# Kernel tuning notes

Hardware: AMD Instinct MI355X
Metric: run time of the kernel (lower is better)

The kernel has to match this reference:

```python
import jax, jax.numpy as jnp
import numpy as np

D_MODEL = 2048
N_HEAD = 16
HEAD_DIM = D_MODEL // N_HEAD


def setup_inputs() -> dict:
    key = jax.random.key(0)
    k1, k2, k3 = jax.random.split(key, 3)
    B, T = 4, 1024
    x = jax.random.normal(k1, (B, T, D_MODEL), dtype=jnp.float32)
    # Linear(d_model, 3*d_model, bias=False): stored as [in, out] for x @ W
    w_qkv = jax.random.normal(k2, (D_MODEL, 3 * D_MODEL), dtype=jnp.float32) * (1.0 / np.sqrt(D_MODEL))
    w_proj = jax.random.normal(k3, (D_MODEL, D_MODEL), dtype=jnp.float32) * (1.0 / np.sqrt(D_MODEL))
    return {"x": x, "w_qkv": w_qkv, "w_proj": w_proj}


def reference(x, w_qkv, w_proj):
    B, T, C = x.shape
    H, Dh = N_HEAD, HEAD_DIM
    qkv = x @ w_qkv                              # [B, T, 3C]
    q, k, v = jnp.split(qkv, 3, axis=-1)
    # [B, T, C] -> [B, H, T, Dh]
    q = q.reshape(B, T, H, Dh).transpose(0, 2, 1, 3)
    k = k.reshape(B, T, H, Dh).transpose(0, 2, 1, 3)
    v = v.reshape(B, T, H, Dh).transpose(0, 2, 1, 3)
    scale = 1.0 / np.sqrt(Dh).astype(np.float32)
    scores = jnp.einsum('bhqd,bhkd->bhqk', q, k) * scale   # [B, H, T, T]
    causal = jnp.tril(jnp.ones((T, T), dtype=bool))
    scores = jnp.where(causal, scores, jnp.finfo(scores.dtype).min)
    attn = jax.nn.softmax(scores, axis=-1)
    y = jnp.einsum('bhqk,bhkd->bhqd', attn, v)             # [B, H, T, Dh]
    y = y.transpose(0, 2, 1, 3).reshape(B, T, C)
    return y @ w_proj
```

## Files before the change

kernel.cpp:

```cpp
#include <hip/hip_runtime.h>
#include <cstdint>
#include <cstddef>


typedef __attribute__((ext_vector_type(8))) __bf16 bf16x8;
typedef __attribute__((ext_vector_type(4))) float f32x4;
typedef unsigned short u16;

#define NEG_BIG (-1.0e30f)

__device__ __forceinline__ u16 f2bf(float f) {
    union { float f; uint32_t u; } v; v.f = f;
    uint32_t r = v.u + 0x7FFFu + ((v.u >> 16) & 1u);
    return (u16)(r >> 16);
}

__device__ __forceinline__ uint32_t pack2(float a, float b) {
    return (uint32_t)f2bf(a) | ((uint32_t)f2bf(b) << 16);
}

__device__ __forceinline__ uint32_t packu(u16 a, u16 b) {
    return (uint32_t)a | ((uint32_t)b << 16);
}

__device__ __forceinline__ f32x4 mfma16(bf16x8 a, bf16x8 b, f32x4 c) {
    return __builtin_amdgcn_mfma_f32_16x16x32_bf16(a, b, c, 0, 0, 0);
}

__device__ __forceinline__ void async16(const u16* g, u16* l) {
    __builtin_amdgcn_global_load_lds(
        (const __attribute__((address_space(1))) void*)g,
        (__attribute__((address_space(3))) void*)l, 16, 0, 0);
}

__global__ __launch_bounds__(256) void cvt_bf16(
    const float* __restrict__ x, u16* __restrict__ xb) {
    size_t i = ((size_t)blockIdx.x * 256 + threadIdx.x) * 8;
    float4 u = *(const float4*)(x + i);
    float4 v = *(const float4*)(x + i + 4);
    uint4 p;
    p.x = pack2(u.x, u.y); p.y = pack2(u.z, u.w);
    p.z = pack2(v.x, v.y); p.w = pack2(v.z, v.w);
    *(uint4*)(xb + i) = p;
}

__global__ __launch_bounds__(256) void transpose_w(
    const float* __restrict__ W, int ldW, u16* __restrict__ WT) {
    __shared__ u16 tile[64][68];
    const int n0 = blockIdx.x * 64, k0 = blockIdx.y * 64;
    const int t = threadIdx.x;
    #pragma unroll
    for (int u = 0; u < 4; ++u) {
        int idx = u * 256 + t;
        int r = idx >> 4, c = (idx & 15) * 4;
        float4 v = *(const float4*)(W + (size_t)(k0 + r) * ldW + n0 + c);
        tile[r][c]     = f2bf(v.x);
        tile[r][c + 1] = f2bf(v.y);
        tile[r][c + 2] = f2bf(v.z);
        tile[r][c + 3] = f2bf(v.w);
    }
    __syncthreads();
    #pragma unroll
    for (int u = 0; u < 2; ++u) {
        int idx = u * 256 + t;
        int r = idx >> 3, ch = (idx & 7) * 8;
        uint4 p;
        p.x = packu(tile[ch][r],     tile[ch + 1][r]);
        p.y = packu(tile[ch + 2][r], tile[ch + 3][r]);
        p.z = packu(tile[ch + 4][r], tile[ch + 5][r]);
        p.w = packu(tile[ch + 6][r], tile[ch + 7][r]);
        *(uint4*)(WT + (size_t)(n0 + r) * 2048 + k0 + ch) = p;
    }
}

__global__ __launch_bounds__(256) void gemm_k(
    const void* __restrict__ Av, const u16* __restrict__ Bt,
    int N, int amode, int omode,
    float* __restrict__ outf, u16* __restrict__ Qo, u16* __restrict__ Ko,
    u16* __restrict__ Vt) {
    const int K = 2048;
    __shared__ u16 As[128][32];
    __shared__ u16 Bs[128][32];

    const float* A32 = (const float*)Av;
    const u16*   A16 = (const u16*)Av;

    const int m0 = blockIdx.y * 128, n0 = blockIdx.x * 128;
    const int t = threadIdx.x;
    const int w = t >> 6, lane = t & 63;
    const int col = lane & 15, quad = lane >> 4;
    const int wrow = (w >> 1) * 64, wcol = (w & 1) * 64;

    f32x4 acc[4][4];
    #pragma unroll
    for (int i = 0; i < 4; ++i)
        #pragma unroll
        for (int j = 0; j < 4; ++j)
            acc[i][j] = (f32x4){0.f, 0.f, 0.f, 0.f};

    u16* as_flat = &As[0][0];
    u16* bs_flat = &Bs[0][0];
    const int c1 = (w << 6) | lane;
    const int c2 = c1 + 256;

    for (int k0 = 0; k0 < K; k0 += 32) {
        {
            const u16* g1 = Bt + (size_t)(n0 + (c1 >> 2)) * K + k0 + ((c1 & 3) << 3);
            async16(g1, bs_flat + (size_t)w * 512);
            const u16* g2 = Bt + (size_t)(n0 + (c2 >> 2)) * K + k0 + ((c2 & 3) << 3);
            async16(g2, bs_flat + 2048 + (size_t)w * 512);
        }
        if (amode == 2) {
            const u16* g1 = A16 + (size_t)(m0 + (c1 >> 2)) * K + k0 + ((c1 & 3) << 3);
            async16(g1, as_flat + (size_t)w * 512);
            const u16* g2 = A16 + (size_t)(m0 + (c2 >> 2)) * K + k0 + ((c2 & 3) << 3);
            async16(g2, as_flat + 2048 + (size_t)w * 512);
        } else if (amode == 1) {
            #pragma unroll
            for (int cc = 0; cc < 2; ++cc) {
                int c = cc ? c2 : c1;
                int r = c >> 2, ko = (c & 3) << 3;
                int kg = k0 + ko, h = kg >> 7, d = kg & 127;
                int m = m0 + r, b = m >> 10, tt = m & 1023;
                const u16* g = A16 + (((size_t)(b * 16 + h)) * 1024 + tt) * 128 + d;
                async16(g, as_flat + (size_t)(cc ? 2048 : 0) + (size_t)w * 512);
            }
        } else if (amode == 0) {
            #pragma unroll
            for (int c = t; c < 512; c += 256) {
                int r = c >> 2, ko = (c & 3) * 8;
                size_t off = (size_t)(m0 + r) * K + k0 + ko;
                float4 u = *(const float4*)(A32 + off);
                float4 v = *(const float4*)(A32 + off + 4);
                uint4 p;
                p.x = pack2(u.x, u.y); p.y = pack2(u.z, u.w);
                p.z = pack2(v.x, v.y); p.w = pack2(v.z, v.w);
                *(uint4*)&As[r][ko] = p;
            }
        } else {
            #pragma unroll
            for (int c = t; c < 512; c += 256) {
                int r = c >> 2, ko = (c & 3) * 8;
                int kg = k0 + ko, h = kg >> 7, d = kg & 127;
                int m = m0 + r, b = m >> 10, tt = m & 1023;
                *(uint4*)&As[r][ko] =
                    *(const uint4*)(A16 + (((size_t)(b * 16 + h)) * 1024 + tt) * 128 + d);
            }
        }
        __syncthreads();

        bf16x8 afr[4], bfr[4];
        #pragma unroll
        for (int i = 0; i < 4; ++i)
            afr[i] = *(const bf16x8*)&As[wrow + i * 16 + col][quad * 8];
        #pragma unroll
        for (int i = 0; i < 4; ++i)
            bfr[i] = *(const bf16x8*)&Bs[wcol + i * 16 + col][quad * 8];

        #pragma unroll
        for (int mt = 0; mt < 4; ++mt)
            #pragma unroll
            for (int nt = 0; nt < 4; ++nt)
                acc[mt][nt] = mfma16(afr[mt], bfr[nt], acc[mt][nt]);
        __syncthreads();
    }

    #pragma unroll
    for (int mt = 0; mt < 4; ++mt) {
        #pragma unroll
        for (int nt = 0; nt < 4; ++nt) {
            #pragma unroll
            for (int r = 0; r < 4; ++r) {
                int gm = m0 + wrow + mt * 16 + quad * 4 + r;
                int gn = n0 + wcol + nt * 16 + col;
                if (omode == 0) {
                    outf[(size_t)gm * N + gn] = acc[mt][nt][r];
                } else {
                    u16 bv = f2bf(acc[mt][nt][r]);
                    int b = gm >> 10, tq = gm & 1023;
                    if (omode == 3) {
                        int which = gn >> 11, rem = gn & 2047;
                        int h = rem >> 7, d = rem & 127;
                        size_t bh = (size_t)b * 16 + h;
                        if (which == 0)      Qo[(bh * 1024 + tq) * 128 + d] = bv;
                        else if (which == 1) Ko[(bh * 1024 + tq) * 128 + d] = bv;
                        else                 Vt[(bh * 128 + d) * 1024 + tq] = bv;
                    } else {
                        int h = gn >> 7, d = gn & 127;
                        size_t bh = (size_t)b * 16 + h;
                        if (omode == 1) Qo[(bh * 1024 + tq) * 128 + d] = bv;
                        else            Vt[(bh * 128 + d) * 1024 + tq] = bv;
                    }
                }
            }
        }
    }
}

__device__ __forceinline__ bf16x8 ldsfrag(const u16* buf, int row, int ksl, int quad) {
    return *(const bf16x8*)(buf + (size_t)row * 64 +
                            ((((ksl << 2) | quad) ^ (row & 7)) << 3));
}

__device__ __forceinline__ void stage64(
    u16* dst, const u16* src, int row0, int k0, int w, int lane) {
    int s = (w << 6) | lane;
    int r = s >> 3;
    int gc = (s & 7) ^ (r & 7);
    async16(src + (size_t)(row0 + r) * 2048 + k0 + (gc << 3),
            dst + ((size_t)(w << 6)) * 8);
}

__global__ __launch_bounds__(512, 2) void gemm192(
    const u16* __restrict__ A, const u16* __restrict__ Bt,
    u16* __restrict__ Qo, u16* __restrict__ Ko, u16* __restrict__ Vt) {
    __shared__ u16 As[2][256 * 64];
    __shared__ u16 Bs[2][192 * 64];

    const int m0 = blockIdx.y * 256, n0 = blockIdx.x * 192;
    const int t = threadIdx.x;
    const int w = t >> 6, lane = t & 63;
    const int col = lane & 15, quad = lane >> 4;
    const int wr16 = ((w >> 2) & 1) << 4;
    const int wc48 = (w & 3) * 48;

    f32x4 acc[8][3];
    #pragma unroll
    for (int i = 0; i < 8; ++i)
        #pragma unroll
        for (int j = 0; j < 3; ++j)
            acc[i][j] = (f32x4){0.f, 0.f, 0.f, 0.f};

    stage64(Bs[0] + 0 * 4096,  Bt, n0 + 0,   0, w, lane);
    stage64(Bs[0] + 1 * 4096,  Bt, n0 + 64,  0, w, lane);
    stage64(Bs[0] + 2 * 4096,  Bt, n0 + 128, 0, w, lane);
    stage64(As[0] + 0 * 4096,  A,  m0 + 0,   0, w, lane);
    stage64(As[0] + 1 * 4096,  A,  m0 + 64,  0, w, lane);
    stage64(As[0] + 2 * 4096,  A,  m0 + 128, 0, w, lane);
    stage64(As[0] + 3 * 4096,  A,  m0 + 192, 0, w, lane);

    bf16x8 af[8], bfc[6];
    const int NT = 32;

    for (int kt = 0; kt < NT; ++kt) {
        const int cur = kt & 1, nxt = cur ^ 1;
        const int kN = ((kt + 1) & 31) * 64;

        asm volatile("s_waitcnt vmcnt(2)" ::: "memory");
        __builtin_amdgcn_s_barrier();
        #pragma unroll
        for (int mr = 0; mr < 4; ++mr)
            #pragma unroll
            for (int ks = 0; ks < 2; ++ks)
                af[mr * 2 + ks] = ldsfrag(As[cur], mr * 32 + wr16 + col, ks, quad);
        #pragma unroll
        for (int nt = 0; nt < 3; ++nt)
            #pragma unroll
            for (int ks = 0; ks < 2; ++ks)
                bfc[nt * 2 + ks] = ldsfrag(Bs[cur], wc48 + nt * 16 + col, ks, quad);
        stage64(Bs[nxt] + 0 * 4096, Bt, n0 + 0,   kN, w, lane);
        stage64(Bs[nxt] + 1 * 4096, Bt, n0 + 64,  kN, w, lane);
        stage64(Bs[nxt] + 2 * 4096, Bt, n0 + 128, kN, w, lane);
        __builtin_amdgcn_s_setprio(1);
        #pragma unroll
        for (int mr = 0; mr < 4; ++mr)
            #pragma unroll
            for (int nt = 0; nt < 3; ++nt)
                #pragma unroll
                for (int ks = 0; ks < 2; ++ks)
                    acc[mr][nt] = mfma16(af[mr * 2 + ks], bfc[nt * 2 + ks], acc[mr][nt]);
        __builtin_amdgcn_s_setprio(0);

        asm volatile("s_waitcnt vmcnt(3)" ::: "memory");
        __builtin_amdgcn_s_barrier();
        #pragma unroll
        for (int mr = 0; mr < 4; ++mr)
            #pragma unroll
            for (int ks = 0; ks < 2; ++ks)
                af[mr * 2 + ks] = ldsfrag(As[cur], (mr + 4) * 32 + wr16 + col, ks, quad);
        stage64(As[nxt] + 0 * 4096, A, m0 + 0,   kN, w, lane);
        stage64(As[nxt] + 1 * 4096, A, m0 + 64,  kN, w, lane);
        stage64(As[nxt] + 2 * 4096, A, m0 + 128, kN, w, lane);
        stage64(As[nxt] + 3 * 4096, A, m0 + 192, kN, w, lane);
        __builtin_amdgcn_s_setprio(1);
        #pragma unroll
        for (int mr = 0; mr < 4; ++mr)
            #pragma unroll
            for (int nt = 0; nt < 3; ++nt)
                #pragma unroll
                for (int ks = 0; ks < 2; ++ks)
                    acc[mr + 4][nt] = mfma16(af[mr * 2 + ks], bfc[nt * 2 + ks], acc[mr + 4][nt]);
        __builtin_amdgcn_s_setprio(0);
    }

    #pragma unroll
    for (int mr = 0; mr < 8; ++mr) {
        #pragma unroll
        for (int nt = 0; nt < 3; ++nt) {
            #pragma unroll
            for (int r = 0; r < 4; ++r) {
                int gm = m0 + mr * 32 + wr16 + quad * 4 + r;
                int gn = n0 + wc48 + nt * 16 + col;
                u16 bv = f2bf(acc[mr][nt][r]);
                int b = gm >> 10, tq = gm & 1023;
                int which = gn >> 11, rem = gn & 2047;
                int hh = rem >> 7, d = rem & 127;
                size_t bh = (size_t)b * 16 + hh;
                if (which == 0)      Qo[(bh * 1024 + tq) * 128 + d] = bv;
                else if (which == 1) Ko[(bh * 1024 + tq) * 128 + d] = bv;
                else                 Vt[(bh * 128 + d) * 1024 + tq] = bv;
            }
        }
    }
}

__global__ __launch_bounds__(256) void attn_kernel(
    u16* __restrict__ Q, const u16* __restrict__ K,
    const u16* __restrict__ VT) {
    __shared__ u16 Ks[64 * 128];
    __shared__ u16 Vs[128 * 64];
    __shared__ u16 Ps[4][16][68];

    const int qb = (int)(gridDim.x - 1) - (int)blockIdx.x;
    const int h = blockIdx.y, b = blockIdx.z;
    const int t = threadIdx.x;
    const int w = t >> 6, lane = t & 63;
    const int col = lane & 15, quad = lane >> 4;
    const int sw = col & 7;
    const size_t bh = (size_t)b * 16 + h;
    u16* Qb = Q + bh * (1024 * 128);
    const u16* Kb = K + bh * (1024 * 128);
    const u16* Vb = VT + bh * (128 * 1024);
    const int q_lane = qb * 64 + w * 16 + col;

    bf16x8 qf[4];
    {
        const u16* qp = Qb + (size_t)q_lane * 128 + quad * 8;
        #pragma unroll
        for (int kq = 0; kq < 4; ++kq)
            qf[kq] = *(const bf16x8*)(qp + kq * 32);
    }

    f32x4 o[8];
    #pragma unroll
    for (int i = 0; i < 8; ++i) o[i] = (f32x4){0.f, 0.f, 0.f, 0.f};
    float m = NEG_BIG, l = 0.f;
    const float scale = 0.08838834764831845f;

    for (int kt = 0; kt <= qb; ++kt) {
        const u16* Kt = Kb + (size_t)kt * (64 * 128);

        #pragma unroll
        for (int i = 0; i < 4; ++i) {
            int s = i * 256 + w * 64 + lane;
            int kr = s >> 4, kc = s & 15;
            async16(Kt + (size_t)kr * 128 + ((kc ^ (kr & 7)) << 3),
                    Ks + (size_t)(i * 256 + w * 64) * 8);
            int vr = s >> 3, vc = s & 7;
            async16(Vb + (size_t)vr * 1024 + kt * 64 + ((vc ^ (vr & 7)) << 3),
                    Vs + (size_t)(i * 256 + w * 64) * 8);
        }
        __syncthreads();

        const bool need_mask = (kt == qb);
        const int ttmax = need_mask ? w : 3;
        f32x4 s[4];
        #pragma unroll
        for (int tt = 0; tt < 4; ++tt) {
            if (tt > ttmax) { s[tt] = (f32x4){NEG_BIG, NEG_BIG, NEG_BIG, NEG_BIG}; continue; }
            const u16* kbase = Ks + (size_t)(tt * 16 + col) * 128;
            f32x4 a = (f32x4){0.f, 0.f, 0.f, 0.f};
            #pragma unroll
            for (int kq = 0; kq < 4; ++kq)
                a = mfma16(*(const bf16x8*)(kbase + (((kq * 4 + quad) ^ sw) << 3)),
                           qf[kq], a);
            s[tt] = a;
        }

        float rmax = NEG_BIG;
        #pragma unroll
        for (int tt = 0; tt < 4; ++tt) {
            if (tt > ttmax) continue;
            #pragma unroll
            for (int r = 0; r < 4; ++r) {
                float v = s[tt][r] * scale;
                int tg = kt * 64 + tt * 16 + quad * 4 + r;
                if (need_mask && tg > q_lane) v = NEG_BIG;
                s[tt][r] = v;
                rmax = fmaxf(rmax, v);
            }
        }
        rmax = fmaxf(rmax, __shfl_xor(rmax, 16, 64));
        rmax = fmaxf(rmax, __shfl_xor(rmax, 32, 64));

        float mnew = fmaxf(m, rmax);
        float alpha = __expf(m - mnew);
        m = mnew;

        float rsum = 0.f;
        #pragma unroll
        for (int tt = 0; tt < 4; ++tt) {
            uint32_t* dst = (uint32_t*)&Ps[w][col][tt * 16 + quad * 4];
            if (tt > ttmax) { dst[0] = 0u; dst[1] = 0u; continue; }
            float p0 = __expf(s[tt][0] - mnew);
            float p1 = __expf(s[tt][1] - mnew);
            float p2 = __expf(s[tt][2] - mnew);
            float p3 = __expf(s[tt][3] - mnew);
            rsum += (p0 + p1) + (p2 + p3);
            dst[0] = pack2(p0, p1);
            dst[1] = pack2(p2, p3);
        }
        rsum += __shfl_xor(rsum, 16, 64);
        rsum += __shfl_xor(rsum, 32, 64);
        l = l * alpha + rsum;

        #pragma unroll
        for (int dt = 0; dt < 8; ++dt)
            #pragma unroll
            for (int r = 0; r < 4; ++r) o[dt][r] *= alpha;

        #pragma unroll
        for (int ks = 0; ks < 2; ++ks) {
            bf16x8 pf = *(const bf16x8*)&Ps[w][col][ks * 32 + quad * 8];
            #pragma unroll
            for (int dt = 0; dt < 8; ++dt) {
                const u16* vbase = Vs + (size_t)(dt * 16 + col) * 64;
                o[dt] = mfma16(*(const bf16x8*)(vbase + (((ks * 4 + quad) ^ sw) << 3)),
                               pf, o[dt]);
            }
        }
        __syncthreads();
    }

    float inv = 1.0f / l;
    #pragma unroll
    for (int dt = 0; dt < 8; ++dt) {
        uint2 p;
        p.x = pack2(o[dt][0] * inv, o[dt][1] * inv);
        p.y = pack2(o[dt][2] * inv, o[dt][3] * inv);
        *(uint2*)&Qb[(size_t)q_lane * 128 + dt * 16 + quad * 4] = p;
    }
}

extern "C" void kernel_launch(void* const* d_in, const int* in_sizes, int n_in,
                              void* d_out, int out_size, void* d_ws, size_t ws_size,
                              hipStream_t stream) {
    const float* x      = (const float*)d_in[0];
    const float* w_qkv  = (const float*)d_in[1];
    const float* w_proj = (const float*)d_in[2];
    float* out = (float*)d_out;

    const size_t SEG = (size_t)4 * 16 * 1024 * 128;
    const size_t NEED_FAST = ((size_t)6144 * 2048 + SEG * 4) * 2;

    if (ws_size >= NEED_FAST + (1u << 20)) {
        u16* wT = (u16*)d_ws;
        u16* xb = wT + (size_t)6144 * 2048;
        u16* Qb = xb + SEG;
        u16* Kb = Qb + SEG;
        u16* Vb = Kb + SEG;

        cvt_bf16<<<4096, 256, 0, stream>>>(x, xb);
        transpose_w<<<dim3(96, 32), 256, 0, stream>>>(w_qkv, 6144, wT);

        gemm192<<<dim3(32, 16), 512, 0, stream>>>(xb, wT, Qb, Kb, Vb);

        attn_kernel<<<dim3(16, 16, 4), 256, 0, stream>>>(Qb, Kb, Vb);

        transpose_w<<<dim3(32, 32), 256, 0, stream>>>(w_proj, 2048, wT);
        gemm_k<<<dim3(16, 32), 256, 0, stream>>>(Qb, wT, 2048, 1, 0,
                                                 out, nullptr, nullptr, nullptr);
    } else {
        u16* wT = (u16*)d_ws;
        u16* Qb = wT + (size_t)2048 * 2048;
        u16* Kb = Qb + SEG;
        u16* Vb = Kb + SEG;

        transpose_w<<<dim3(32, 32), 256, 0, stream>>>(w_qkv + 0, 6144, wT);
        gemm_k<<<dim3(16, 32), 256, 0, stream>>>(x, wT, 2048, 0, 1,
                                                 nullptr, Qb, nullptr, nullptr);
        transpose_w<<<dim3(32, 32), 256, 0, stream>>>(w_qkv + 2048, 6144, wT);
        gemm_k<<<dim3(16, 32), 256, 0, stream>>>(x, wT, 2048, 0, 1,
                                                 nullptr, Kb, nullptr, nullptr);
        transpose_w<<<dim3(32, 32), 256, 0, stream>>>(w_qkv + 4096, 6144, wT);
        gemm_k<<<dim3(16, 32), 256, 0, stream>>>(x, wT, 2048, 0, 2,
                                                 nullptr, nullptr, nullptr, Vb);

        attn_kernel<<<dim3(16, 16, 4), 256, 0, stream>>>(Qb, Kb, Vb);

        transpose_w<<<dim3(32, 32), 256, 0, stream>>>(w_proj, 2048, wT);
        gemm_k<<<dim3(16, 32), 256, 0, stream>>>(Qb, wT, 2048, 3, 0,
                                                 out, nullptr, nullptr, nullptr);
    }
}
```

Measured before the change: 436.2 us.

## Software-pipeline LDS fragment reads ahead of MFMAs in QKV GEMM

Restructures the QKV GEMM main loop into a two-k-tile unrolled schedule with double-buffered register fragments (aX/aY, bX/bY). Each half-tile's LDS reads for the next half are issued before the current half's MFMAs, so LDS latency overlaps with matrix work. The cost is higher VGPR pressure from the duplicated fragment arrays. The weight-transpose kernel is also changed from vectorized float4/uint4 accesses to scalar element loops, which is likely slower but it is a small one-time kernel.

```diff
diff --git a/kernel.cpp b/kernel.cpp
--- a/kernel.cpp
+++ b/kernel.cpp
@@ -17,10 +17,6 @@
 
 __device__ __forceinline__ uint32_t pack2(float a, float b) {
     return (uint32_t)f2bf(a) | ((uint32_t)f2bf(b) << 16);
-}
-
-__device__ __forceinline__ uint32_t packu(u16 a, u16 b) {
-    return (uint32_t)a | ((uint32_t)b << 16);
 }
 
 __device__ __forceinline__ f32x4 mfma16(bf16x8 a, bf16x8 b, f32x4 c) {
@@ -49,27 +45,14 @@
     __shared__ u16 tile[64][68];
     const int n0 = blockIdx.x * 64, k0 = blockIdx.y * 64;
     const int t = threadIdx.x;
-    #pragma unroll
-    for (int u = 0; u < 4; ++u) {
-        int idx = u * 256 + t;
-        int r = idx >> 4, c = (idx & 15) * 4;
-        float4 v = *(const float4*)(W + (size_t)(k0 + r) * ldW + n0 + c);
-        tile[r][c]     = f2bf(v.x);
-        tile[r][c + 1] = f2bf(v.y);
-        tile[r][c + 2] = f2bf(v.z);
-        tile[r][c + 3] = f2bf(v.w);
+    for (int i = t; i < 4096; i += 256) {
+        int r = i >> 6, c = i & 63;
+        tile[r][c] = f2bf(W[(size_t)(k0 + r) * ldW + n0 + c]);
     }
     __syncthreads();
-    #pragma unroll
-    for (int u = 0; u < 2; ++u) {
-        int idx = u * 256 + t;
-        int r = idx >> 3, ch = (idx & 7) * 8;
-        uint4 p;
-        p.x = packu(tile[ch][r],     tile[ch + 1][r]);
-        p.y = packu(tile[ch + 2][r], tile[ch + 3][r]);
-        p.z = packu(tile[ch + 4][r], tile[ch + 5][r]);
-        p.w = packu(tile[ch + 6][r], tile[ch + 7][r]);
-        *(uint4*)(WT + (size_t)(n0 + r) * 2048 + k0 + ch) = p;
+    for (int i = t; i < 4096; i += 256) {
+        int r = i >> 6, c = i & 63;
+        WT[(size_t)(n0 + r) * 2048 + k0 + c] = tile[c][r];
     }
 }
 
@@ -211,6 +194,53 @@
             dst + ((size_t)(w << 6)) * 8);
 }
 
+__device__ __forceinline__ void stageB3(u16* buf, const u16* Bt, int n0,
+                                        int k0, int w, int lane) {
+    stage64(buf + 0 * 4096, Bt, n0 + 0,   k0, w, lane);
+    stage64(buf + 1 * 4096, Bt, n0 + 64,  k0, w, lane);
+    stage64(buf + 2 * 4096, Bt, n0 + 128, k0, w, lane);
+}
+
+__device__ __forceinline__ void stageA4(u16* buf, const u16* A, int m0,
+                                        int k0, int w, int lane) {
+    stage64(buf + 0 * 4096, A, m0 + 0,   k0, w, lane);
+    stage64(buf + 1 * 4096, A, m0 + 64,  k0, w, lane);
+    stage64(buf + 2 * 4096, A, m0 + 128, k0, w, lane);
+    stage64(buf + 3 * 4096, A, m0 + 192, k0, w, lane);
+}
+
+__device__ __forceinline__ void read_a192(bf16x8* af, const u16* buf, int mh,
+                                          int wr16, int col, int quad) {
+    #pragma unroll
+    for (int mr = 0; mr < 4; ++mr)
+        #pragma unroll
+        for (int ks = 0; ks < 2; ++ks)
+            af[mr * 2 + ks] = ldsfrag(buf, (mh * 4 + mr) * 32 + wr16 + col, ks, quad);
+}
+
+__device__ __forceinline__ void read_b192(bf16x8* bf, const u16* buf,
+                                          int wc48, int col, int quad) {
+    #pragma unroll
+    for (int nt = 0; nt < 3; ++nt)
+        #pragma unroll
+        for (int ks = 0; ks < 2; ++ks)
+            bf[nt * 2 + ks] = ldsfrag(buf, wc48 + nt * 16 + col, ks, quad);
+}
+
+__device__ __forceinline__ void mfma24(f32x4 (&acc)[8][3], int mh,
+                                       const bf16x8* af, const bf16x8* bf) {
+    __builtin_amdgcn_s_setprio(1);
+    #pragma unroll
+    for (int mr = 0; mr < 4; ++mr)
+        #pragma unroll
+        for (int nt = 0; nt < 3; ++nt)
+            #pragma unroll
+            for (int ks = 0; ks < 2; ++ks)
+                acc[mh * 4 + mr][nt] = mfma16(af[mr * 2 + ks], bf[nt * 2 + ks],
+                                              acc[mh * 4 + mr][nt]);
+    __builtin_amdgcn_s_setprio(0);
+}
+
 __global__ __launch_bounds__(512, 2) void gemm192(
     const u16* __restrict__ A, const u16* __restrict__ Bt,
     u16* __restrict__ Qo, u16* __restrict__ Ko, u16* __restrict__ Vt) {
@@ -231,66 +261,44 @@
         for (int j = 0; j < 3; ++j)
             acc[i][j] = (f32x4){0.f, 0.f, 0.f, 0.f};
 
-    stage64(Bs[0] + 0 * 4096,  Bt, n0 + 0,   0, w, lane);
-    stage64(Bs[0] + 1 * 4096,  Bt, n0 + 64,  0, w, lane);
-    stage64(Bs[0] + 2 * 4096,  Bt, n0 + 128, 0, w, lane);
-    stage64(As[0] + 0 * 4096,  A,  m0 + 0,   0, w, lane);
-    stage64(As[0] + 1 * 4096,  A,  m0 + 64,  0, w, lane);
-    stage64(As[0] + 2 * 4096,  A,  m0 + 128, 0, w, lane);
-    stage64(As[0] + 3 * 4096,  A,  m0 + 192, 0, w, lane);
-
-    bf16x8 af[8], bfc[6];
-    const int NT = 32;
-
-    for (int kt = 0; kt < NT; ++kt) {
-        const int cur = kt & 1, nxt = cur ^ 1;
-        const int kN = ((kt + 1) & 31) * 64;
-
+    stageB3(Bs[0], Bt, n0, 0, w, lane);
+    stageA4(As[0], A,  m0, 0, w, lane);
+    asm volatile("s_waitcnt vmcnt(2)" ::: "memory");
+    __builtin_amdgcn_s_barrier();
+
+    bf16x8 aX[8], aY[8], bX[6], bY[6];
+    read_a192(aX, As[0], 0, wr16, col, quad);
+    read_b192(bX, Bs[0], wc48, col, quad);
+
+    for (int it = 0; it < 16; ++it) {
+        const int k1 = (2 * it + 1) & 31;
+        const int k2 = (2 * it + 2) & 31;
+
+        stageB3(Bs[1], Bt, n0, k1 * 64, w, lane);
+        asm volatile("s_waitcnt vmcnt(3)" ::: "memory");
+        __builtin_amdgcn_s_barrier();
+        read_a192(aY, As[0], 1, wr16, col, quad);
+        mfma24(acc, 0, aX, bX);
+
+        stageA4(As[1], A, m0, k1 * 64, w, lane);
         asm volatile("s_waitcnt vmcnt(2)" ::: "memory");
         __builtin_amdgcn_s_barrier();
-        #pragma unroll
-        for (int mr = 0; mr < 4; ++mr)
-            #pragma unroll
-            for (int ks = 0; ks < 2; ++ks)
-                af[mr * 2 + ks] = ldsfrag(As[cur], mr * 32 + wr16 + col, ks, quad);
-        #pragma unroll
-        for (int nt = 0; nt < 3; ++nt)
-            #pragma unroll
-            for (int ks = 0; ks < 2; ++ks)
-                bfc[nt * 2 + ks] = ldsfrag(Bs[cur], wc48 + nt * 16 + col, ks, quad);
-        stage64(Bs[nxt] + 0 * 4096, Bt, n0 + 0,   kN, w, lane);
-        stage64(Bs[nxt] + 1 * 4096, Bt, n0 + 64,  kN, w, lane);
-        stage64(Bs[nxt] + 2 * 4096, Bt, n0 + 128, kN, w, lane);
-        __builtin_amdgcn_s_setprio(1);
-        #pragma unroll
-        for (int mr = 0; mr < 4; ++mr)
-            #pragma unroll
-            for (int nt = 0; nt < 3; ++nt)
-                #pragma unroll
-                for (int ks = 0; ks < 2; ++ks)
-                    acc[mr][nt] = mfma16(af[mr * 2 + ks], bfc[nt * 2 + ks], acc[mr][nt]);
-        __builtin_amdgcn_s_setprio(0);
-
+        read_a192(aX, As[1], 0, wr16, col, quad);
+        read_b192(bY, Bs[1], wc48, col, quad);
+        mfma24(acc, 1, aY, bX);
+
+        stageB3(Bs[0], Bt, n0, k2 * 64, w, lane);
         asm volatile("s_waitcnt vmcnt(3)" ::: "memory");
         __builtin_amdgcn_s_barrier();
-        #pragma unroll
-        for (int mr = 0; mr < 4; ++mr)
-            #pragma unroll
-            for (int ks = 0; ks < 2; ++ks)
-                af[mr * 2 + ks] = ldsfrag(As[cur], (mr + 4) * 32 + wr16 + col, ks, quad);
-        stage64(As[nxt] + 0 * 4096, A, m0 + 0,   kN, w, lane);
-        stage64(As[nxt] + 1 * 4096, A, m0 + 64,  kN, w, lane);
-        stage64(As[nxt] + 2 * 4096, A, m0 + 128, kN, w, lane);
-        stage64(As[nxt] + 3 * 4096, A, m0 + 192, kN, w, lane);
-        __builtin_amdgcn_s_setprio(1);
-        #pragma unroll
-        for (int mr = 0; mr < 4; ++mr)
-            #pragma unroll
-            for (int nt = 0; nt < 3; ++nt)
-                #pragma unroll
-                for (int ks = 0; ks < 2; ++ks)
-                    acc[mr + 4][nt] = mfma16(af[mr * 2 + ks], bfc[nt * 2 + ks], acc[mr + 4][nt]);
-        __builtin_amdgcn_s_setprio(0);
+        read_a192(aY, As[1], 1, wr16, col, quad);
+        mfma24(acc, 0, aX, bY);
+
+        stageA4(As[0], A, m0, k2 * 64, w, lane);
+        asm volatile("s_waitcnt vmcnt(2)" ::: "memory");
+        __builtin_amdgcn_s_barrier();
+        read_a192(aX, As[0], 0, wr16, col, quad);
+        read_b192(bX, Bs[0], wc48, col, quad);
+        mfma24(acc, 1, aY, bY);
     }
 
     #pragma unroll
```

After: 442.9 us. Within noise of the previous version (+1.5%).

## Register-prefetch next K/V tile in attention; simplify weight transpose

Applied to the files above, without the earlier changes.

The attention kernel now loads the next K/V tile from global memory into registers while the current tile is being computed, then writes the registers to LDS at the start of the following iteration. This replaces the direct global-to-LDS async loads and is meant to hide global load latency behind the MFMA work. The weight transpose kernel is also simplified to scalar element loads and stores, which gives up its vectorized float4 and uint4 accesses. The prefetch adds register pressure, and it is unclear whether the loop has a barrier before LDS is overwritten that avoids a race.

```diff
diff --git a/kernel.cpp b/kernel.cpp
--- a/kernel.cpp
+++ b/kernel.cpp
@@ -17,10 +17,6 @@
 
 __device__ __forceinline__ uint32_t pack2(float a, float b) {
     return (uint32_t)f2bf(a) | ((uint32_t)f2bf(b) << 16);
-}
-
-__device__ __forceinline__ uint32_t packu(u16 a, u16 b) {
-    return (uint32_t)a | ((uint32_t)b << 16);
 }
 
 __device__ __forceinline__ f32x4 mfma16(bf16x8 a, bf16x8 b, f32x4 c) {
@@ -49,27 +45,14 @@
     __shared__ u16 tile[64][68];
     const int n0 = blockIdx.x * 64, k0 = blockIdx.y * 64;
     const int t = threadIdx.x;
-    #pragma unroll
-    for (int u = 0; u < 4; ++u) {
-        int idx = u * 256 + t;
-        int r = idx >> 4, c = (idx & 15) * 4;
-        float4 v = *(const float4*)(W + (size_t)(k0 + r) * ldW + n0 + c);
-        tile[r][c]     = f2bf(v.x);
-        tile[r][c + 1] = f2bf(v.y);
-        tile[r][c + 2] = f2bf(v.z);
-        tile[r][c + 3] = f2bf(v.w);
+    for (int i = t; i < 4096; i += 256) {
+        int r = i >> 6, c = i & 63;
+        tile[r][c] = f2bf(W[(size_t)(k0 + r) * ldW + n0 + c]);
     }
     __syncthreads();
-    #pragma unroll
-    for (int u = 0; u < 2; ++u) {
-        int idx = u * 256 + t;
-        int r = idx >> 3, ch = (idx & 7) * 8;
-        uint4 p;
-        p.x = packu(tile[ch][r],     tile[ch + 1][r]);
-        p.y = packu(tile[ch + 2][r], tile[ch + 3][r]);
-        p.z = packu(tile[ch + 4][r], tile[ch + 5][r]);
-        p.w = packu(tile[ch + 6][r], tile[ch + 7][r]);
-        *(uint4*)(WT + (size_t)(n0 + r) * 2048 + k0 + ch) = p;
+    for (int i = t; i < 4096; i += 256) {
+        int r = i >> 6, c = i & 63;
+        WT[(size_t)(n0 + r) * 2048 + k0 + c] = tile[c][r];
     }
 }
 
@@ -332,6 +315,7 @@
     const u16* Kb = K + bh * (1024 * 128);
     const u16* Vb = VT + bh * (128 * 1024);
     const int q_lane = qb * 64 + w * 16 + col;
+    const int s0 = w * 64 + lane;
 
     bf16x8 qf[4];
     {
@@ -347,20 +331,37 @@
     float m = NEG_BIG, l = 0.f;
     const float scale = 0.08838834764831845f;
 
+    uint4 kreg[4], vreg[4];
+    #pragma unroll
+    for (int i = 0; i < 4; ++i) {
+        int s = i * 256 + s0;
+        int kr = s >> 4, kc = s & 15;
+        kreg[i] = *(const uint4*)(Kb + (size_t)kr * 128 + ((kc ^ (kr & 7)) << 3));
+        int vr = s >> 3, vc = s & 7;
+        vreg[i] = *(const uint4*)(Vb + (size_t)vr * 1024 + ((vc ^ (vr & 7)) << 3));
+    }
+
     for (int kt = 0; kt <= qb; ++kt) {
-        const u16* Kt = Kb + (size_t)kt * (64 * 128);
-
         #pragma unroll
         for (int i = 0; i < 4; ++i) {
-            int s = i * 256 + w * 64 + lane;
-            int kr = s >> 4, kc = s & 15;
-            async16(Kt + (size_t)kr * 128 + ((kc ^ (kr & 7)) << 3),
-                    Ks + (size_t)(i * 256 + w * 64) * 8);
-            int vr = s >> 3, vc = s & 7;
-            async16(Vb + (size_t)vr * 1024 + kt * 64 + ((vc ^ (vr & 7)) << 3),
-                    Vs + (size_t)(i * 256 + w * 64) * 8);
+            int s = i * 256 + s0;
+            *(uint4*)(Ks + (size_t)s * 8) = kreg[i];
+            *(uint4*)(Vs + (size_t)s * 8) = vreg[i];
         }
         __syncthreads();
+
+        if (kt < qb) {
+            const u16* Kt = Kb + (size_t)(kt + 1) * (64 * 128);
+            const int kvoff = (kt + 1) * 64;
+            #pragma unroll
+            for (int i = 0; i < 4; ++i) {
+                int s = i * 256 + s0;
+                int kr = s >> 4, kc = s & 15;
+                kreg[i] = *(const uint4*)(Kt + (size_t)kr * 128 + ((kc ^ (kr & 7)) << 3));
+                int vr = s >> 3, vc = s & 7;
+                vreg[i] = *(const uint4*)(Vb + (size_t)vr * 1024 + kvoff + ((vc ^ (vr & 7)) << 3));
+            }
+        }
 
         const bool need_mask = (kt == qb);
         const int ttmax = need_mask ? w : 3;
```

Measured after the change: 489.7 us. 12.2% more time.

## Pair causal query blocks per attention workgroup and simplify weight transpose

Applied to the files above, without the earlier changes.

Each attention workgroup now handles two query blocks, 15-bx and bx, one after the other, so every block does the same total number of KV tiles. The grid is halved from 16 to 8 in x. This is meant to remove the causal load imbalance and tail effect, at the cost of fewer resident workgroups (512) and serialized work per block. Separately, the weight transpose kernel is rewritten to use scalar loads and stores instead of float4/uint4 vectors, which is likely slower on its own.

```diff
diff --git a/kernel.cpp b/kernel.cpp
--- a/kernel.cpp
+++ b/kernel.cpp
@@ -17,10 +17,6 @@
 
 __device__ __forceinline__ uint32_t pack2(float a, float b) {
     return (uint32_t)f2bf(a) | ((uint32_t)f2bf(b) << 16);
-}
-
-__device__ __forceinline__ uint32_t packu(u16 a, u16 b) {
-    return (uint32_t)a | ((uint32_t)b << 16);
 }
 
 __device__ __forceinline__ f32x4 mfma16(bf16x8 a, bf16x8 b, f32x4 c) {
@@ -49,27 +45,14 @@
     __shared__ u16 tile[64][68];
     const int n0 = blockIdx.x * 64, k0 = blockIdx.y * 64;
     const int t = threadIdx.x;
-    #pragma unroll
-    for (int u = 0; u < 4; ++u) {
-        int idx = u * 256 + t;
-        int r = idx >> 4, c = (idx & 15) * 4;
-        float4 v = *(const float4*)(W + (size_t)(k0 + r) * ldW + n0 + c);
-        tile[r][c]     = f2bf(v.x);
-        tile[r][c + 1] = f2bf(v.y);
-        tile[r][c + 2] = f2bf(v.z);
-        tile[r][c + 3] = f2bf(v.w);
+    for (int i = t; i < 4096; i += 256) {
+        int r = i >> 6, c = i & 63;
+        tile[r][c] = f2bf(W[(size_t)(k0 + r) * ldW + n0 + c]);
     }
     __syncthreads();
-    #pragma unroll
-    for (int u = 0; u < 2; ++u) {
-        int idx = u * 256 + t;
-        int r = idx >> 3, ch = (idx & 7) * 8;
-        uint4 p;
-        p.x = packu(tile[ch][r],     tile[ch + 1][r]);
-        p.y = packu(tile[ch + 2][r], tile[ch + 3][r]);
-        p.z = packu(tile[ch + 4][r], tile[ch + 5][r]);
-        p.w = packu(tile[ch + 6][r], tile[ch + 7][r]);
-        *(uint4*)(WT + (size_t)(n0 + r) * 2048 + k0 + ch) = p;
+    for (int i = t; i < 4096; i += 256) {
+        int r = i >> 6, c = i & 63;
+        WT[(size_t)(n0 + r) * 2048 + k0 + c] = tile[c][r];
     }
 }
 
@@ -321,7 +304,7 @@
     __shared__ u16 Vs[128 * 64];
     __shared__ u16 Ps[4][16][68];
 
-    const int qb = (int)(gridDim.x - 1) - (int)blockIdx.x;
+    const int bx = (int)blockIdx.x;
     const int h = blockIdx.y, b = blockIdx.z;
     const int t = threadIdx.x;
     const int w = t >> 6, lane = t & 63;
@@ -331,114 +314,119 @@
     u16* Qb = Q + bh * (1024 * 128);
     const u16* Kb = K + bh * (1024 * 128);
     const u16* Vb = VT + bh * (128 * 1024);
-    const int q_lane = qb * 64 + w * 16 + col;
-
-    bf16x8 qf[4];
-    {
-        const u16* qp = Qb + (size_t)q_lane * 128 + quad * 8;
-        #pragma unroll
-        for (int kq = 0; kq < 4; ++kq)
-            qf[kq] = *(const bf16x8*)(qp + kq * 32);
-    }
-
-    f32x4 o[8];
-    #pragma unroll
-    for (int i = 0; i < 8; ++i) o[i] = (f32x4){0.f, 0.f, 0.f, 0.f};
-    float m = NEG_BIG, l = 0.f;
     const float scale = 0.08838834764831845f;
 
-    for (int kt = 0; kt <= qb; ++kt) {
-        const u16* Kt = Kb + (size_t)kt * (64 * 128);
-
-        #pragma unroll
-        for (int i = 0; i < 4; ++i) {
-            int s = i * 256 + w * 64 + lane;
-            int kr = s >> 4, kc = s & 15;
-            async16(Kt + (size_t)kr * 128 + ((kc ^ (kr & 7)) << 3),
-                    Ks + (size_t)(i * 256 + w * 64) * 8);
-            int vr = s >> 3, vc = s & 7;
-            async16(Vb + (size_t)vr * 1024 + kt * 64 + ((vc ^ (vr & 7)) << 3),
-                    Vs + (size_t)(i * 256 + w * 64) * 8);
-        }
-        __syncthreads();
-
-        const bool need_mask = (kt == qb);
-        const int ttmax = need_mask ? w : 3;
-        f32x4 s[4];
-        #pragma unroll
-        for (int tt = 0; tt < 4; ++tt) {
-            if (tt > ttmax) { s[tt] = (f32x4){NEG_BIG, NEG_BIG, NEG_BIG, NEG_BIG}; continue; }
-            const u16* kbase = Ks + (size_t)(tt * 16 + col) * 128;
-            f32x4 a = (f32x4){0.f, 0.f, 0.f, 0.f};
+    #pragma unroll 1
+    for (int qs = 0; qs < 2; ++qs) {
+        const int qb = qs ? bx : 15 - bx;
+        const int q_lane = qb * 64 + w * 16 + col;
+
+        bf16x8 qf[4];
+        {
+            const u16* qp = Qb + (size_t)q_lane * 128 + quad * 8;
             #pragma unroll
             for (int kq = 0; kq < 4; ++kq)
-                a = mfma16(*(const bf16x8*)(kbase + (((kq * 4 + quad) ^ sw) << 3)),
-                           qf[kq], a);
-            s[tt] = a;
-        }
-
-        float rmax = NEG_BIG;
-        #pragma unroll
-        for (int tt = 0; tt < 4; ++tt) {
-            if (tt > ttmax) continue;
-            #pragma unroll
-            for (int r = 0; r < 4; ++r) {
-                float v = s[tt][r] * scale;
-                int tg = kt * 64 + tt * 16 + quad * 4 + r;
-                if (need_mask && tg > q_lane) v = NEG_BIG;
-                s[tt][r] = v;
-                rmax = fmaxf(rmax, v);
-            }
-        }
-        rmax = fmaxf(rmax, __shfl_xor(rmax, 16, 64));
-        rmax = fmaxf(rmax, __shfl_xor(rmax, 32, 64));
-
-        float mnew = fmaxf(m, rmax);
-        float alpha = __expf(m - mnew);
-        m = mnew;
-
-        float rsum = 0.f;
-        #pragma unroll
-        for (int tt = 0; tt < 4; ++tt) {
-            uint32_t* dst = (uint32_t*)&Ps[w][col][tt * 16 + quad * 4];
-            if (tt > ttmax) { dst[0] = 0u; dst[1] = 0u; continue; }
-            float p0 = __expf(s[tt][0] - mnew);
-            float p1 = __expf(s[tt][1] - mnew);
-            float p2 = __expf(s[tt][2] - mnew);
-            float p3 = __expf(s[tt][3] - mnew);
-            rsum += (p0 + p1) + (p2 + p3);
-            dst[0] = pack2(p0, p1);
-            dst[1] = pack2(p2, p3);
-        }
-        rsum += __shfl_xor(rsum, 16, 64);
-        rsum += __shfl_xor(rsum, 32, 64);
-        l = l * alpha + rsum;
-
-        #pragma unroll
-        for (int dt = 0; dt < 8; ++dt)
-            #pragma unroll
-            for (int r = 0; r < 4; ++r) o[dt][r] *= alpha;
-
-        #pragma unroll
-        for (int ks = 0; ks < 2; ++ks) {
-            bf16x8 pf = *(const bf16x8*)&Ps[w][col][ks * 32 + quad * 8];
-            #pragma unroll
-            for (int dt = 0; dt < 8; ++dt) {
-                const u16* vbase = Vs + (size_t)(dt * 16 + col) * 64;
-                o[dt] = mfma16(*(const bf16x8*)(vbase + (((ks * 4 + quad) ^ sw) << 3)),
-                               pf, o[dt]);
-            }
-        }
-        __syncthreads();
-    }
-
-    float inv = 1.0f / l;
-    #pragma unroll
-    for (int dt = 0; dt < 8; ++dt) {
-        uint2 p;
-        p.x = pack2(o[dt][0] * inv, o[dt][1] * inv);
-        p.y = pack2(o[dt][2] * inv, o[dt][3] * inv);
-        *(uint2*)&Qb[(size_t)q_lane * 128 + dt * 16 + quad * 4] = p;
+                qf[kq] = *(const bf16x8*)(qp + kq * 32);
+        }
+
+        f32x4 o[8];
+        #pragma unroll
+        for (int i = 0; i < 8; ++i) o[i] = (f32x4){0.f, 0.f, 0.f, 0.f};
+        float m = NEG_BIG, l = 0.f;
+
+        for (int kt = 0; kt <= qb; ++kt) {
+            const u16* Kt = Kb + (size_t)kt * (64 * 128);
+
+            #pragma unroll
+            for (int i = 0; i < 4; ++i) {
+                int s = i * 256 + w * 64 + lane;
+                int kr = s >> 4, kc = s & 15;
+                async16(Kt + (size_t)kr * 128 + ((kc ^ (kr & 7)) << 3),
+                        Ks + (size_t)(i * 256 + w * 64) * 8);
+                int vr = s >> 3, vc = s & 7;
+                async16(Vb + (size_t)vr * 1024 + kt * 64 + ((vc ^ (vr & 7)) << 3),
+                        Vs + (size_t)(i * 256 + w * 64) * 8);
+            }
+            __syncthreads();
+
+            const bool need_mask = (kt == qb);
+            const int ttmax = need_mask ? w : 3;
+            f32x4 s[4];
+            #pragma unroll
+            for (int tt = 0; tt < 4; ++tt) {
+                if (tt > ttmax) { s[tt] = (f32x4){NEG_BIG, NEG_BIG, NEG_BIG, NEG_BIG}; continue; }
+                const u16* kbase = Ks + (size_t)(tt * 16 + col) * 128;
+                f32x4 a = (f32x4){0.f, 0.f, 0.f, 0.f};
+                #pragma unroll
+                for (int kq = 0; kq < 4; ++kq)
+                    a = mfma16(*(const bf16x8*)(kbase + (((kq * 4 + quad) ^ sw) << 3)),
+                               qf[kq], a);
+                s[tt] = a;
+            }
+
+            float rmax = NEG_BIG;
+            #pragma unroll
+            for (int tt = 0; tt < 4; ++tt) {
+                if (tt > ttmax) continue;
+                #pragma unroll
+                for (int r = 0; r < 4; ++r) {
+                    float v = s[tt][r] * scale;
+                    int tg = kt * 64 + tt * 16 + quad * 4 + r;
+                    if (need_mask && tg > q_lane) v = NEG_BIG;
+                    s[tt][r] = v;
+                    rmax = fmaxf(rmax, v);
+                }
+            }
+            rmax = fmaxf(rmax, __shfl_xor(rmax, 16, 64));
+            rmax = fmaxf(rmax, __shfl_xor(rmax, 32, 64));
+
+            float mnew = fmaxf(m, rmax);
+            float alpha = __expf(m - mnew);
+            m = mnew;
+
+            float rsum = 0.f;
+            #pragma unroll
+            for (int tt = 0; tt < 4; ++tt) {
+                uint32_t* dst = (uint32_t*)&Ps[w][col][tt * 16 + quad * 4];
+                if (tt > ttmax) { dst[0] = 0u; dst[1] = 0u; continue; }
+                float p0 = __expf(s[tt][0] - mnew);
+                float p1 = __expf(s[tt][1] - mnew);
+                float p2 = __expf(s[tt][2] - mnew);
+                float p3 = __expf(s[tt][3] - mnew);
+                rsum += (p0 + p1) + (p2 + p3);
+                dst[0] = pack2(p0, p1);
+                dst[1] = pack2(p2, p3);
+            }
+            rsum += __shfl_xor(rsum, 16, 64);
+            rsum += __shfl_xor(rsum, 32, 64);
+            l = l * alpha + rsum;
+
+            #pragma unroll
+            for (int dt = 0; dt < 8; ++dt)
+                #pragma unroll
+                for (int r = 0; r < 4; ++r) o[dt][r] *= alpha;
+
+            #pragma unroll
+            for (int ks = 0; ks < 2; ++ks) {
+                bf16x8 pf = *(const bf16x8*)&Ps[w][col][ks * 32 + quad * 8];
+                #pragma unroll
+                for (int dt = 0; dt < 8; ++dt) {
+                    const u16* vbase = Vs + (size_t)(dt * 16 + col) * 64;
+                    o[dt] = mfma16(*(const bf16x8*)(vbase + (((ks * 4 + quad) ^ sw) << 3)),
+                                   pf, o[dt]);
+                }
+            }
+            __syncthreads();
+        }
+
+        float inv = 1.0f / l;
+        #pragma unroll
+        for (int dt = 0; dt < 8; ++dt) {
+            uint2 p;
+            p.x = pack2(o[dt][0] * inv, o[dt][1] * inv);
+            p.y = pack2(o[dt][2] * inv, o[dt][3] * inv);
+            *(uint2*)&Qb[(size_t)q_lane * 128 + dt * 16 + quad * 4] = p;
+        }
     }
 }
 
@@ -465,7 +453,7 @@
 
         gemm192<<<dim3(32, 16), 512, 0, stream>>>(xb, wT, Qb, Kb, Vb);
 
-        attn_kernel<<<dim3(16, 16, 4), 256, 0, stream>>>(Qb, Kb, Vb);
+        attn_kernel<<<dim3(8, 16, 4), 256, 0, stream>>>(Qb, Kb, Vb);
 
         transpose_w<<<dim3(32, 32), 256, 0, stream>>>(w_proj, 2048, wT);
         gemm_k<<<dim3(16, 32), 256, 0, stream>>>(Qb, wT, 2048, 1, 0,
@@ -486,7 +474,7 @@
         gemm_k<<<dim3(16, 32), 256, 0, stream>>>(x, wT, 2048, 0, 2,
                                                  nullptr, nullptr, nullptr, Vb);
 
-        attn_kernel<<<dim3(16, 16, 4), 256, 0, stream>>>(Qb, Kb, Vb);
+        attn_kernel<<<dim3(8, 16, 4), 256, 0, stream>>>(Qb, Kb, Vb);
 
         transpose_w<<<dim3(32, 32), 256, 0, stream>>>(w_proj, 2048, wT);
         gemm_k<<<dim3(16, 32), 256, 0, stream>>>(Qb, wT, 2048, 3, 0,
```

Measured after the change: 372.6 us. 1.17x faster.
